# Kernel tuning notes

Hardware: AMD Instinct MI355X
Metric: run time of the kernel (lower is better)

## Reference

```python
import jax, jax.numpy as jnp
import numpy as np

HARD_NUM = 700      # hardcoded self.hard_num in HardOIMLoss
OIM_SCALAR = 30.0   # oim_scalar init arg
N, D, P, Q = 4096, 256, 5532, 5000


def _l2norm(x):
    return x / jnp.linalg.norm(x, axis=-1, keepdims=True)


def setup_inputs() -> dict:
    key = jax.random.key(0)
    k1, k2, k3, k4, k5 = jax.random.split(key, 5)
    # OIM features and lookup tables are L2-normalized rows
    inputs = _l2norm(jax.random.normal(k1, (N, D), dtype=jnp.float32))
    lut = _l2norm(jax.random.normal(k2, (P, D), dtype=jnp.float32))
    cq = _l2norm(jax.random.normal(k3, (Q, D), dtype=jnp.float32))
    reliability = jax.random.uniform(k4, (P + Q,), dtype=jnp.float32)
    labels = jax.random.randint(k5, (N,), 0, P, dtype=jnp.int32)
    return {"inputs": inputs, "labels": labels, "lut": lut, "cq": cq,
            "reliability": reliability}


def reference(inputs, labels, lut, cq, reliability):
    # projected[n, c] = <inputs_n, table_c> * reliability_c ;  table = [lut; cq]
    table = jnp.concatenate([lut, cq], axis=0)            # [P+Q, D]
    projected = (inputs @ table.T) * reliability[None, :]  # [N, P+Q]
    C = projected.shape[1]
    # value at sorted-descending index HARD_NUM == (HARD_NUM+1)-th largest
    boundary = jax.lax.top_k(projected, HARD_NUM + 1)[0][:, -1]  # [N]
    hard_mask = projected >= boundary[:, None]
    label_mask = jnp.arange(C, dtype=labels.dtype)[None, :] == labels[:, None]
    mask = hard_mask | label_mask
    logits = jnp.where(mask, projected * OIM_SCALAR, -jnp.inf)
    # cross entropy (mean over rows); label column is always unmasked
    logZ = jax.scipy.special.logsumexp(logits, axis=1)
    tgt = jnp.take_along_axis(logits, labels[:, None].astype(jnp.int32), axis=1)[:, 0]
    return jnp.mean(logZ - tgt)
```

## Files before the change

### kernel.cpp

```cpp
#include <hip/hip_runtime.h>
#include <math.h>

#define N_ROWS 4096
#define DIM    256
#define P_SZ   5532
#define Q_SZ   5000
#define C_COLS 10532
#define TPAD   10624
#define PSTR   10624
#define NGR    (PSTR / 16)
#define K_SEL  701
#define SCALAR 30.0f
#define C2     (SCALAR * 1.4426950408889634f)

typedef __attribute__((ext_vector_type(8))) short   short8;
typedef __attribute__((ext_vector_type(4))) float   float4_t;
typedef __attribute__((ext_vector_type(4))) unsigned short ushort4_t;
typedef __attribute__((ext_vector_type(8))) unsigned short ushort8_t;
typedef __attribute__((ext_vector_type(4))) unsigned int  uint4_t;

__device__ __forceinline__ unsigned short f2bf(float f) {
    unsigned u = __float_as_uint(f);
    unsigned r = u + 0x7FFFu + ((u >> 16) & 1u);
    return (unsigned short)(r >> 16);
}
__device__ __forceinline__ float bf2f(unsigned short u) {
    return __uint_as_float((unsigned)u << 16);
}
__device__ __forceinline__ unsigned short key16(unsigned short u) {
    return (u & 0x8000u) ? (unsigned short)(~u) : (unsigned short)(u | 0x8000u);
}
__device__ __forceinline__ float key2f16(unsigned key) {
    unsigned short b = (key & 0x8000u) ? (unsigned short)(key & 0x7FFFu)
                                       : (unsigned short)(~key & 0xFFFFu);
    return bf2f(b);
}
__device__ __forceinline__ void gload16(const void* g, void* l) {
    __builtin_amdgcn_global_load_lds(
        (const __attribute__((address_space(1))) unsigned int*)g,
        (__attribute__((address_space(3))) unsigned int*)l, 16, 0, 0);
}

#define NIN_G  (N_ROWS * DIM / 4)
#define NTAB_G (TPAD * DIM / 4)

__global__ __launch_bounds__(256) void convert_bf16(
    const float* __restrict__ inputs, const float* __restrict__ lut,
    const float* __restrict__ cq, unsigned short* __restrict__ in_bf,
    unsigned short* __restrict__ tab_bf)
{
    const int g = blockIdx.x * 256 + threadIdx.x;
    if (g >= NIN_G + NTAB_G) return;
    float4_t v;
    unsigned short* dst;
    if (g < NIN_G) {
        v = *(const float4_t*)&inputs[(size_t)g * 4];
        dst = in_bf + (size_t)g * 4;
    } else {
        const int t = g - NIN_G;
        const int row = t >> 6;
        const int c4  = (t & 63) * 4;
        if (row < P_SZ)        v = *(const float4_t*)&lut[(size_t)row * DIM + c4];
        else if (row < C_COLS) v = *(const float4_t*)&cq[(size_t)(row - P_SZ) * DIM + c4];
        else                   v = (float4_t){0.f, 0.f, 0.f, 0.f};
        dst = tab_bf + (size_t)t * 4;
    }
    ushort4_t h = { f2bf(v.x), f2bf(v.y), f2bf(v.z), f2bf(v.w) };
    *(ushort4_t*)dst = h;
}

#define NWG_X 83
#define NWG_Y 32
#define NWG   (NWG_X * NWG_Y)
#define CSTR  132

__global__ __launch_bounds__(256) void gemm_proj(
    const unsigned short* __restrict__ in_bf,
    const unsigned short* __restrict__ tab_bf,
    const float* __restrict__ rel,
    unsigned short* __restrict__ proj)
{
    __shared__ __align__(16) unsigned short smem[128 * CSTR];
    unsigned short* At = smem;
    unsigned short* Bt = smem + 128 * 64;

    const int tid  = threadIdx.x;
    const int lane = tid & 63, wid = tid >> 6;
    const int wm = wid >> 1, wn = wid & 1;

    const int phys = blockIdx.x;
    const int wg   = (phys & 7) * (NWG / 8) + (phys >> 3);
    const int bx   = wg >> 5;
    const int by   = wg & 31;
    const int row0 = by * 128, col0 = bx * 128;

    float4_t acc[4][4];
    #pragma unroll
    for (int i = 0; i < 4; ++i)
        #pragma unroll
        for (int j = 0; j < 4; ++j)
            acc[i][j] = (float4_t){0.f, 0.f, 0.f, 0.f};

    for (int k0 = 0; k0 < DIM; k0 += 64) {
        #pragma unroll
        for (int it = 0; it < 4; ++it) {
            const int g  = it * 256 + tid;
            const int r  = g >> 3;
            const int kb = ((g & 7) * 16) ^ ((r & 7) << 4);
            gload16(in_bf  + (size_t)(row0 + r) * DIM + k0 + (kb >> 1),
                    (char*)At + g * 16);
            gload16(tab_bf + (size_t)(col0 + r) * DIM + k0 + (kb >> 1),
                    (char*)Bt + g * 16);
        }
        __syncthreads();

        #pragma unroll
        for (int kk = 0; kk < 2; ++kk) {
            const int krow = lane & 15;
            const int kb   = kk * 64 + ((lane >> 4) << 4);
            short8 af[4], bfr[4];
            #pragma unroll
            for (int i = 0; i < 4; ++i) {
                const int r = wm * 64 + i * 16 + krow;
                af[i] = *(const short8*)((const char*)At + (r * 128 + (kb ^ ((r & 7) << 4))));
            }
            #pragma unroll
            for (int j = 0; j < 4; ++j) {
                const int r = wn * 64 + j * 16 + krow;
                bfr[j] = *(const short8*)((const char*)Bt + (r * 128 + (kb ^ ((r & 7) << 4))));
            }
            #pragma unroll
            for (int i = 0; i < 4; ++i)
                #pragma unroll
                for (int j = 0; j < 4; ++j)
                    acc[i][j] = __builtin_amdgcn_mfma_f32_16x16x32_bf16(af[i], bfr[j], acc[i][j], 0, 0, 0);
        }
        __syncthreads();
    }

    const int lr = (lane >> 4) << 2;
    const int lc = lane & 15;
    #pragma unroll
    for (int j = 0; j < 4; ++j) {
        const int cl  = wn * 64 + j * 16 + lc;
        const int col = col0 + cl;
        const bool pad = (col >= C_COLS);
        const float rl = pad ? 0.f : rel[col];
        #pragma unroll
        for (int i = 0; i < 4; ++i) {
            const int rbase = wm * 64 + i * 16 + lr;
            #pragma unroll
            for (int rr = 0; rr < 4; ++rr)
                smem[(rbase + rr) * CSTR + cl] =
                    pad ? (unsigned short)0u : key16(f2bf(acc[i][j][rr] * rl));
        }
    }
    __syncthreads();
    #pragma unroll
    for (int it = 0; it < 8; ++it) {
        const int g = it * 256 + tid;
        const int r = g >> 4;
        const int c8 = (g & 15) * 8;
        *(ushort8_t*)(proj + (size_t)(row0 + r) * PSTR + col0 + c8) =
            *(const ushort8_t*)&smem[r * CSTR + c8];
    }
}

#define SCAP  32
__global__ __launch_bounds__(256) void row_loss_kernel(
    const unsigned short* __restrict__ proj, const int* __restrict__ labels,
    float* __restrict__ row_loss)
{
    __shared__ unsigned short stash[SCAP * 256];
    __shared__ unsigned h2[256];
    __shared__ unsigned wsum[2][4];
    __shared__ float    fsum[4];
    __shared__ unsigned sel_sub, ovf;

    const int tid = threadIdx.x, lane = tid & 63, wid = tid >> 6;
    const int row = blockIdx.x;
    const uint4_t* prow = (const uint4_t*)(proj + (size_t)row * PSTR);

    h2[tid] = 0;
    if (tid == 0) ovf = 0;

    const int tailv = (1280 + tid < NGR);
    uint4_t r0 = prow[tid];
    uint4_t r1 = prow[256 + tid];
    uint4_t r2 = prow[512 + tid];
    uint4_t r3 = prow[768 + tid];
    uint4_t r4 = prow[1024 + tid];
    uint4_t r5 = prow[tailv ? 1280 + tid : 1279];

    unsigned lo = 0, hi = 256, cnt_hi = 0;
    for (int pass = 0; pass < 8; ++pass) {
        const unsigned mid = (lo + hi) >> 1;
        const unsigned hiT = mid << 24;
        unsigned c = 0;
        auto CW = [&](unsigned w) {
            c += (w >= hiT) ? 1u : 0u;
            c += ((w << 16) >= hiT) ? 1u : 0u;
        };
        #pragma unroll
        for (int d = 0; d < 4; ++d) CW(r0[d]);
        #pragma unroll
        for (int d = 0; d < 4; ++d) CW(r1[d]);
        #pragma unroll
        for (int d = 0; d < 4; ++d) CW(r2[d]);
        #pragma unroll
        for (int d = 0; d < 4; ++d) CW(r3[d]);
        #pragma unroll
        for (int d = 0; d < 4; ++d) CW(r4[d]);
        if (tailv) {
            #pragma unroll
            for (int d = 0; d < 4; ++d) CW(r5[d]);
        }
        #pragma unroll
        for (int off = 1; off < 64; off <<= 1) {
            const unsigned t = __shfl_down(c, off, 64);
            if (lane + off < 64) c += t;
        }
        if (lane == 0) wsum[pass & 1][wid] = c;
        __syncthreads();
        const unsigned total = wsum[pass & 1][0] + wsum[pass & 1][1]
                             + wsum[pass & 1][2] + wsum[pass & 1][3];
        if (total >= K_SEL) lo = mid;
        else { hi = mid; cnt_hi = total; }
    }
    const unsigned b1 = lo;
    const unsigned k2 = K_SEL - cnt_hi;
    const unsigned kfloor = b1 << 8;
    const unsigned kceil  = kfloor + 256u;

    unsigned cnt = 0;
    auto ST = [&](unsigned key) {
        if (key >= kfloor) {
            if (cnt < SCAP) stash[cnt * 256 + tid] = (unsigned short)key;
            else ovf = 1u;
            ++cnt;
        }
    };
    auto SW = [&](uint4_t w) {
        #pragma unroll
        for (int d = 0; d < 4; ++d) { ST(w[d] & 0xFFFFu); ST(w[d] >> 16); }
    };
    SW(r0); SW(r1); SW(r2); SW(r3); SW(r4);
    if (tailv) SW(r5);
    __syncthreads();

    float s = 0.f;
    unsigned bkey;
    if (ovf == 0) {
        for (unsigned c = 0; c < cnt; ++c) {
            const unsigned key = stash[c * 256 + tid];
            if (key < kceil) atomicAdd(&h2[key & 0xFFu], 1u);
        }
        __syncthreads();
        {
            const unsigned c = h2[tid];
            unsigned incl = c;
            #pragma unroll
            for (int off = 1; off < 64; off <<= 1) {
                const unsigned t = __shfl_down(incl, off, 64);
                if (lane + off < 64) incl += t;
            }
            if (lane == 0) wsum[0][wid] = incl;
            __syncthreads();
            unsigned above = incl - c;
            for (int w = wid + 1; w < 4; ++w) above += wsum[0][w];
            if (above < k2 && above + c >= k2) sel_sub = (unsigned)tid;
        }
        __syncthreads();
        bkey = kfloor | sel_sub;
        for (unsigned c = 0; c < cnt; ++c) {
            const unsigned key = stash[c * 256 + tid];
            if (key >= bkey) s += exp2f(C2 * key2f16(key) - C2);
        }
    } else {
        auto SB = [&](unsigned w) {
            const unsigned lv = w & 0xFFFFu, hv = w >> 16;
            if ((lv >> 8) == b1) atomicAdd(&h2[lv & 0xFFu], 1u);
            if ((hv >> 8) == b1) atomicAdd(&h2[hv & 0xFFu], 1u);
        };
        #pragma unroll
        for (int d = 0; d < 4; ++d) SB(r0[d]);
        #pragma unroll
        for (int d = 0; d < 4; ++d) SB(r1[d]);
        #pragma unroll
        for (int d = 0; d < 4; ++d) SB(r2[d]);
        #pragma unroll
        for (int d = 0; d < 4; ++d) SB(r3[d]);
        #pragma unroll
        for (int d = 0; d < 4; ++d) SB(r4[d]);
        if (tailv) {
            #pragma unroll
            for (int d = 0; d < 4; ++d) SB(r5[d]);
        }
        __syncthreads();
        {
            const unsigned c = h2[tid];
            unsigned incl = c;
            #pragma unroll
            for (int off = 1; off < 64; off <<= 1) {
                const unsigned t = __shfl_down(incl, off, 64);
                if (lane + off < 64) incl += t;
            }
            if (lane == 0) wsum[0][wid] = incl;
            __syncthreads();
            unsigned above = incl - c;
            for (int w = wid + 1; w < 4; ++w) above += wsum[0][w];
            if (above < k2 && above + c >= k2) sel_sub = (unsigned)tid;
        }
        __syncthreads();
        bkey = kfloor | sel_sub;
        auto EX = [&](unsigned w) {
            const unsigned lv = w & 0xFFFFu, hv = w >> 16;
            if (lv >= bkey) s += exp2f(C2 * key2f16(lv) - C2);
            if (hv >= bkey) s += exp2f(C2 * key2f16(hv) - C2);
        };
        #pragma unroll
        for (int d = 0; d < 4; ++d) EX(r0[d]);
        #pragma unroll
        for (int d = 0; d < 4; ++d) EX(r1[d]);
        #pragma unroll
        for (int d = 0; d < 4; ++d) EX(r2[d]);
        #pragma unroll
        for (int d = 0; d < 4; ++d) EX(r3[d]);
        #pragma unroll
        for (int d = 0; d < 4; ++d) EX(r4[d]);
        if (tailv) {
            #pragma unroll
            for (int d = 0; d < 4; ++d) EX(r5[d]);
        }
    }

    #pragma unroll
    for (int off = 1; off < 64; off <<= 1) {
        const float t = __shfl_down(s, off, 64);
        if (lane + off < 64) s += t;
    }
    if (lane == 0) fsum[wid] = s;
    __syncthreads();

    if (tid == 0) {
        float total = fsum[0] + fsum[1] + fsum[2] + fsum[3];
        const unsigned ulk = ((const unsigned short*)prow)[labels[row]];
        const float pl = key2f16(ulk);
        if (ulk < bkey) total += exp2f(C2 * pl - C2);
        row_loss[row] = SCALAR * 1.0f + logf(total) - SCALAR * pl;
    }
}

__global__ __launch_bounds__(256) void final_reduce(
    const float* __restrict__ row_loss, float* __restrict__ out)
{
    __shared__ float fred[4];
    const int tid = threadIdx.x, lane = tid & 63, wid = tid >> 6;
    float s = 0.f;
    for (int i = tid; i < N_ROWS; i += 256) s += row_loss[i];
    #pragma unroll
    for (int off = 1; off < 64; off <<= 1) {
        const float t = __shfl_down(s, off, 64);
        if (lane + off < 64) s += t;
    }
    if (lane == 0) fred[wid] = s;
    __syncthreads();
    if (tid == 0) out[0] = (fred[0] + fred[1] + fred[2] + fred[3]) / (float)N_ROWS;
}

extern "C" void kernel_launch(void* const* d_in, const int* in_sizes, int n_in,
                              void* d_out, int out_size, void* d_ws, size_t ws_size,
                              hipStream_t stream) {
    const float* inputs = (const float*)d_in[0];
    const int*   labels = (const int*)d_in[1];
    const float* lut    = (const float*)d_in[2];
    const float* cq     = (const float*)d_in[3];
    const float* rel    = (const float*)d_in[4];
    float* out = (float*)d_out;

    unsigned short* in_bf  = (unsigned short*)d_ws;
    unsigned short* tab_bf = in_bf  + (size_t)N_ROWS * DIM;
    unsigned short* proj   = tab_bf + (size_t)TPAD * DIM;
    float* rl_buf = (float*)(proj + (size_t)N_ROWS * PSTR);

    convert_bf16<<<(NIN_G + NTAB_G) / 256, 256, 0, stream>>>(inputs, lut, cq, in_bf, tab_bf);
    gemm_proj<<<NWG, 256, 0, stream>>>(in_bf, tab_bf, rel, proj);
    row_loss_kernel<<<N_ROWS, 256, 0, stream>>>(proj, labels, rl_buf);
    final_reduce<<<1, 256, 0, stream>>>(rl_buf, out);
}
```

Before: 97.42 us.

## Double-buffer GEMM K-loop with async loads and use ballot counts in radix select

The projection GEMM now splits K into eight 32-wide steps with two LDS buffers. The next tile's global-to-LDS loads are issued before computing on the current one, using explicit vmcnt waits and raw barriers, so load latency overlaps the MFMA work. Separately, the per-pass threshold count in the row-loss kernel uses wave ballots plus popcount instead of per-lane counters and a shuffle reduction. The pipeline depends on a hand-tuned vmcnt value and barrier placement being correct, and the ballot version issues more scalar/ballot operations per element.

Result: no change. 96.30 us (median of 4 runs) (-1.1%).

```diff
diff --git a/kernel.cpp b/kernel.cpp
--- a/kernel.cpp
+++ b/kernel.cpp
@@ -81,8 +81,6 @@
     unsigned short* __restrict__ proj)
 {
     __shared__ __align__(16) unsigned short smem[128 * CSTR];
-    unsigned short* At = smem;
-    unsigned short* Bt = smem + 128 * 64;
 
     const int tid  = threadIdx.x;
     const int lane = tid & 63, wid = tid >> 6;
@@ -101,41 +99,51 @@
         for (int j = 0; j < 4; ++j)
             acc[i][j] = (float4_t){0.f, 0.f, 0.f, 0.f};
 
-    for (int k0 = 0; k0 < DIM; k0 += 64) {
-        #pragma unroll
-        for (int it = 0; it < 4; ++it) {
+    auto STAGE = [&](int b, int k0) {
+        #pragma unroll
+        for (int it = 0; it < 2; ++it) {
             const int g  = it * 256 + tid;
-            const int r  = g >> 3;
-            const int kb = ((g & 7) * 16) ^ ((r & 7) << 4);
+            const int r  = g >> 2;
+            const int kb = ((g & 3) * 16) ^ ((r & 3) << 4);
             gload16(in_bf  + (size_t)(row0 + r) * DIM + k0 + (kb >> 1),
-                    (char*)At + g * 16);
+                    (char*)smem + b * 8192 + g * 16);
             gload16(tab_bf + (size_t)(col0 + r) * DIM + k0 + (kb >> 1),
-                    (char*)Bt + g * 16);
-        }
-        __syncthreads();
-
-        #pragma unroll
-        for (int kk = 0; kk < 2; ++kk) {
-            const int krow = lane & 15;
-            const int kb   = kk * 64 + ((lane >> 4) << 4);
-            short8 af[4], bfr[4];
-            #pragma unroll
-            for (int i = 0; i < 4; ++i) {
-                const int r = wm * 64 + i * 16 + krow;
-                af[i] = *(const short8*)((const char*)At + (r * 128 + (kb ^ ((r & 7) << 4))));
-            }
-            #pragma unroll
-            for (int j = 0; j < 4; ++j) {
-                const int r = wn * 64 + j * 16 + krow;
-                bfr[j] = *(const short8*)((const char*)Bt + (r * 128 + (kb ^ ((r & 7) << 4))));
-            }
-            #pragma unroll
-            for (int i = 0; i < 4; ++i)
-                #pragma unroll
-                for (int j = 0; j < 4; ++j)
-                    acc[i][j] = __builtin_amdgcn_mfma_f32_16x16x32_bf16(af[i], bfr[j], acc[i][j], 0, 0, 0);
-        }
-        __syncthreads();
+                    (char*)smem + 16384 + b * 8192 + g * 16);
+        }
+    };
+
+    STAGE(0, 0);
+    #pragma unroll
+    for (int t = 0; t < 8; ++t) {
+        if (t < 7) {
+            STAGE((t + 1) & 1, (t + 1) * 32);
+            asm volatile("s_waitcnt vmcnt(4)" ::: "memory");
+        } else {
+            asm volatile("s_waitcnt vmcnt(0)" ::: "memory");
+        }
+        __builtin_amdgcn_s_barrier();
+
+        const char* At = (const char*)smem + (t & 1) * 8192;
+        const char* Bt = (const char*)smem + 16384 + (t & 1) * 8192;
+        const int krow = lane & 15;
+        const int kb   = (lane >> 4) << 4;
+        short8 af[4], bfr[4];
+        #pragma unroll
+        for (int i = 0; i < 4; ++i) {
+            const int r = wm * 64 + i * 16 + krow;
+            af[i] = *(const short8*)(At + r * 64 + (kb ^ ((r & 3) << 4)));
+        }
+        #pragma unroll
+        for (int j = 0; j < 4; ++j) {
+            const int r = wn * 64 + j * 16 + krow;
+            bfr[j] = *(const short8*)(Bt + r * 64 + (kb ^ ((r & 3) << 4)));
+        }
+        #pragma unroll
+        for (int i = 0; i < 4; ++i)
+            #pragma unroll
+            for (int j = 0; j < 4; ++j)
+                acc[i][j] = __builtin_amdgcn_mfma_f32_16x16x32_bf16(af[i], bfr[j], acc[i][j], 0, 0, 0);
+        __builtin_amdgcn_s_barrier();
     }
 
     const int lr = (lane >> 4) << 2;
@@ -184,7 +192,7 @@
     h2[tid] = 0;
     if (tid == 0) ovf = 0;
 
-    const int tailv = (1280 + tid < NGR);
+    const bool tailv = (1280 + tid < NGR);
     uint4_t r0 = prow[tid];
     uint4_t r1 = prow[256 + tid];
     uint4_t r2 = prow[512 + tid];
@@ -197,28 +205,24 @@
         const unsigned mid = (lo + hi) >> 1;
         const unsigned hiT = mid << 24;
         unsigned c = 0;
-        auto CW = [&](unsigned w) {
-            c += (w >= hiT) ? 1u : 0u;
-            c += ((w << 16) >= hiT) ? 1u : 0u;
+        auto CB = [&](unsigned w) {
+            c += (unsigned)__popcll(__ballot(w >= hiT));
+            c += (unsigned)__popcll(__ballot((w << 16) >= hiT));
         };
         #pragma unroll
-        for (int d = 0; d < 4; ++d) CW(r0[d]);
-        #pragma unroll
-        for (int d = 0; d < 4; ++d) CW(r1[d]);
-        #pragma unroll
-        for (int d = 0; d < 4; ++d) CW(r2[d]);
-        #pragma unroll
-        for (int d = 0; d < 4; ++d) CW(r3[d]);
-        #pragma unroll
-        for (int d = 0; d < 4; ++d) CW(r4[d]);
-        if (tailv) {
-            #pragma unroll
-            for (int d = 0; d < 4; ++d) CW(r5[d]);
-        }
-        #pragma unroll
-        for (int off = 1; off < 64; off <<= 1) {
-            const unsigned t = __shfl_down(c, off, 64);
-            if (lane + off < 64) c += t;
+        for (int d = 0; d < 4; ++d) CB(r0[d]);
+        #pragma unroll
+        for (int d = 0; d < 4; ++d) CB(r1[d]);
+        #pragma unroll
+        for (int d = 0; d < 4; ++d) CB(r2[d]);
+        #pragma unroll
+        for (int d = 0; d < 4; ++d) CB(r3[d]);
+        #pragma unroll
+        for (int d = 0; d < 4; ++d) CB(r4[d]);
+        #pragma unroll
+        for (int d = 0; d < 4; ++d) {
+            c += (unsigned)__popcll(__ballot(tailv && (r5[d] >= hiT)));
+            c += (unsigned)__popcll(__ballot(tailv && ((r5[d] << 16) >= hiT)));
         }
         if (lane == 0) wsum[pass & 1][wid] = c;
         __syncthreads();
```
